# Performance work log

Measured on AMD Instinct MI355X. Metric: run time of the kernel, lower is better.

## Reference

```python
import jax, jax.numpy as jnp
import numpy as np
import math

N_HEAD = 16
N_EMBD = 1024
N_LATENTS = 64
HEAD_DIM = N_EMBD // N_HEAD  # 64
ROPE_THETA = 10000.0


def setup_inputs() -> dict:
    key = jax.random.key(0)
    ks = jax.random.split(key, 6)
    B, T = 4, 4096
    x = jax.random.normal(ks[0], (B, T, N_EMBD), dtype=jnp.float32)
    # torch Linear weights applied as x @ W with W: [in, out] (equivalent up to init)
    s = 1.0 / math.sqrt(N_EMBD)
    Wk = jax.random.normal(ks[1], (N_EMBD, N_EMBD), dtype=jnp.float32) * s
    Wv = jax.random.normal(ks[2], (N_EMBD, N_EMBD), dtype=jnp.float32) * s
    Wg = jax.random.normal(ks[3], (N_EMBD, N_HEAD * N_LATENTS), dtype=jnp.float32) * s
    Wp = jax.random.normal(ks[4], (N_EMBD, N_EMBD), dtype=jnp.float32) * s
    latent_q = jax.random.normal(ks[5], (1, N_LATENTS, N_HEAD, HEAD_DIM), dtype=jnp.float32)
    return {"x": x, "latent_q": latent_q, "Wk": Wk, "Wv": Wv, "Wg": Wg, "Wp": Wp}


def _rope_interleaved(k, theta):
    # k: [B, T, H, D]; interleaved pairs rotated by position-dependent angles
    B, T, H, D = k.shape
    inv_freq = 1.0 / (theta ** (jnp.arange(0, D, 2, dtype=jnp.float32) / D))  # [D/2]
    ang = jnp.arange(T, dtype=jnp.float32)[:, None] * inv_freq[None, :]       # [T, D/2]
    cos = jnp.cos(ang)[None, :, None, :]
    sin = jnp.sin(ang)[None, :, None, :]
    k2 = k.reshape(B, T, H, D // 2, 2)
    kr = jnp.stack([k2[..., 0] * cos - k2[..., 1] * sin,
                    k2[..., 0] * sin + k2[..., 1] * cos], axis=-1)
    return kr.reshape(B, T, H, D).astype(k.dtype)


def reference(x, latent_q, Wk, Wv, Wg, Wp):
    B, T, C = x.shape
    H, D, L = N_HEAD, HEAD_DIM, N_LATENTS
    k = (x @ Wk).reshape(B, T, H, D)
    v = (x @ Wv).reshape(B, T, H, D)
    gates = jax.nn.softmax((x @ Wg).reshape(B, T, H, L), axis=-1)  # [B,T,H,L]
    k = _rope_interleaved(k, ROPE_THETA)
    q = jnp.broadcast_to(latent_q, (B, L, H, D)).transpose(0, 2, 1, 3)  # [B,H,L,D]
    kt = k.transpose(0, 2, 1, 3)  # [B,H,T,D]
    vt = v.transpose(0, 2, 1, 3)  # [B,H,T,D]
    scale = 1.0 / jnp.sqrt(jnp.asarray(D, dtype=x.dtype))
    scores = jnp.einsum('bhld,bhtd->bhlt', q, kt) * scale  # [B,H,L,T]
    # PyTorch SDPA is_causal with L_q != L_kv: top-left aligned tril(ones(L, T))
    causal = jnp.arange(T)[None, :] <= jnp.arange(L)[:, None]  # [L,T]
    scores = jnp.where(causal[None, None], scores, -jnp.inf)
    attn = jax.nn.softmax(scores, axis=-1)
    attn_out = jnp.einsum('bhlt,bhtd->bhld', attn, vt)  # [B,H,L,D]
    gates_t = gates.transpose(0, 2, 1, 3)  # [B,H,T,L]
    weighted = jnp.einsum('bhld,bhtl->bhtd', attn_out, gates_t)  # [B,H,T,D]
    out = weighted.transpose(0, 2, 1, 3).reshape(B, T, C)
    return out @ Wp
```

## Files before the change

### kernel.cpp

```cpp
#include <hip/hip_runtime.h>
#include <hip/hip_bf16.h>


typedef __attribute__((ext_vector_type(8))) short bf16x8;
typedef __attribute__((ext_vector_type(4))) float f32x4;
typedef __attribute__((ext_vector_type(4))) unsigned short us4;

__device__ __forceinline__ void gll16(const void* g, void* l) {
  __builtin_amdgcn_global_load_lds((const __attribute__((address_space(1))) void*)g,
                                   (__attribute__((address_space(3))) void*)l, 16, 0, 0);
}

__global__ __launch_bounds__(256)
void prep_kernel(const float* __restrict__ x, __hip_bfloat16* __restrict__ xb,
                 const float* __restrict__ Wg, const float* __restrict__ Wk,
                 const float* __restrict__ Wv, const float* __restrict__ Wp,
                 __hip_bfloat16* __restrict__ WgT, __hip_bfloat16* __restrict__ WkT,
                 __hip_bfloat16* __restrict__ WvT, __hip_bfloat16* __restrict__ WpT) {
  const int bid = blockIdx.x, tid = threadIdx.x;
  if (bid < 2048) {
    const int stride = 2048 * 256;
    for (int i = bid * 256 + tid; i < 4194304; i += stride) {
      float4 f = reinterpret_cast<const float4*>(x)[i];
      union { __hip_bfloat16 h[4]; us4 v; } u;
      u.h[0] = __float2bfloat16(f.x);
      u.h[1] = __float2bfloat16(f.y);
      u.h[2] = __float2bfloat16(f.z);
      u.h[3] = __float2bfloat16(f.w);
      reinterpret_cast<us4*>(xb)[i] = u.v;
    }
  } else {
    const int t = bid - 2048;
    const int z = t >> 10, rem = t & 1023;
    const float* W = (z == 0) ? Wg : ((z == 1) ? Wk : ((z == 2) ? Wv : Wp));
    __hip_bfloat16* Wt = (z == 0) ? WgT : ((z == 1) ? WkT : ((z == 2) ? WvT : WpT));
    __shared__ float tile[32][33];
    const int bx = (rem & 31) * 32, by = (rem >> 5) * 32;
    const int tx = tid & 31, ty = tid >> 5;
    #pragma unroll
    for (int j = 0; j < 32; j += 8)
      tile[ty + j][tx] = W[(size_t)(by + ty + j) * 1024 + bx + tx];
    __syncthreads();
    #pragma unroll
    for (int j = 0; j < 32; j += 8)
      Wt[(size_t)(bx + ty + j) * 1024 + by + tx] = __float2bfloat16(tile[tx][ty + j]);
  }
}

template <int EPI>
__global__ __launch_bounds__(512, 2)
void gemm256(const __hip_bfloat16* __restrict__ A, const __hip_bfloat16* __restrict__ Bt,
             void* __restrict__ Cv, int K, int ldc,
             long long astride, long long bstride, long long cstride) {
  __shared__ __align__(16) unsigned short SA[2][256 * 64];
  __shared__ __align__(16) unsigned short SB[2][256 * 64];
  const int tid = threadIdx.x;
  const int lane = tid & 63;
  const int w = tid >> 6;
  const int wm = w >> 2, wn = w & 3;
  const int lr = lane & 15, lk = lane >> 4;
  const int m0 = blockIdx.x * 256, n0 = blockIdx.y * 256;
  const long long b = blockIdx.z;
  const __hip_bfloat16* Ab = A + b * astride;
  const __hip_bfloat16* Bb = Bt + b * bstride;

  f32x4 acc[8][4] = {};

  const int NT = K >> 6;
  int buf = 0;

  auto STAGE = [&](int bsel, int kt) {
    #pragma unroll
    for (int r = 0; r < 4; ++r) {
      int c = r * 512 + tid;
      int row = c >> 3, slot = c & 7;
      int gch = slot ^ (row & 7);
      gll16(Ab + (size_t)(m0 + row) * K + kt + gch * 8, (char*)&SA[bsel][0] + c * 16);
      gll16(Bb + (size_t)(n0 + row) * K + kt + gch * 8, (char*)&SB[bsel][0] + c * 16);
    }
  };

  STAGE(0, 0);
  __syncthreads();

  for (int t = 0; t < NT; ++t) {
    if (t + 1 < NT) STAGE(buf ^ 1, (t + 1) << 6);

    bf16x8 bfr[2][4];
    #pragma unroll
    for (int kk = 0; kk < 2; ++kk)
      #pragma unroll
      for (int ni = 0; ni < 4; ++ni) {
        int row = wn * 64 + ni * 16 + lr;
        int ch = (kk * 4 + lk) ^ (row & 7);
        bfr[kk][ni] = *(const bf16x8*)&SB[buf][row * 64 + ch * 8];
      }
    #pragma unroll
    for (int mi = 0; mi < 8; ++mi) {
      int row = wm * 128 + mi * 16 + lr;
      int ch0 = lk ^ (row & 7);
      int ch1 = (4 + lk) ^ (row & 7);
      bf16x8 a0 = *(const bf16x8*)&SA[buf][row * 64 + ch0 * 8];
      bf16x8 a1 = *(const bf16x8*)&SA[buf][row * 64 + ch1 * 8];
      #pragma unroll
      for (int ni = 0; ni < 4; ++ni)
        acc[mi][ni] = __builtin_amdgcn_mfma_f32_16x16x32_bf16(a0, bfr[0][ni], acc[mi][ni], 0, 0, 0);
      #pragma unroll
      for (int ni = 0; ni < 4; ++ni)
        acc[mi][ni] = __builtin_amdgcn_mfma_f32_16x16x32_bf16(a1, bfr[1][ni], acc[mi][ni], 0, 0, 0);
    }
    __syncthreads();
    buf ^= 1;
  }

  if (EPI == 0) {
    float* C = (float*)Cv + b * cstride;
    #pragma unroll
    for (int mi = 0; mi < 8; ++mi) {
      int r = m0 + wm * 128 + mi * 16 + lk * 4;
      #pragma unroll
      for (int ni = 0; ni < 4; ++ni) {
        int c = n0 + wn * 64 + ni * 16 + lr;
        #pragma unroll
        for (int jj = 0; jj < 4; ++jj)
          C[(size_t)(r + jj) * ldc + c] = acc[mi][ni][jj];
      }
    }
  } else {
    __hip_bfloat16* C = (__hip_bfloat16*)Cv + b * cstride;
    #pragma unroll
    for (int mi = 0; mi < 8; ++mi) {
      #pragma unroll
      for (int jj = 0; jj < 4; ++jj) {
        float mx = -3.0e38f;
        #pragma unroll
        for (int ni = 0; ni < 4; ++ni) mx = fmaxf(mx, acc[mi][ni][jj]);
        mx = fmaxf(mx, __shfl_xor(mx, 1));
        mx = fmaxf(mx, __shfl_xor(mx, 2));
        mx = fmaxf(mx, __shfl_xor(mx, 4));
        mx = fmaxf(mx, __shfl_xor(mx, 8));
        float e[4];
        float s = 0.f;
        #pragma unroll
        for (int ni = 0; ni < 4; ++ni) { e[ni] = __expf(acc[mi][ni][jj] - mx); s += e[ni]; }
        s += __shfl_xor(s, 1);
        s += __shfl_xor(s, 2);
        s += __shfl_xor(s, 4);
        s += __shfl_xor(s, 8);
        float inv = 1.0f / s;
        int r = m0 + wm * 128 + mi * 16 + lk * 4 + jj;
        #pragma unroll
        for (int ni = 0; ni < 4; ++ni)
          C[(size_t)r * ldc + n0 + wn * 64 + ni * 16 + lr] = __float2bfloat16(e[ni] * inv);
      }
    }
  }
}

__global__ __launch_bounds__(256)
void gemm_kv(const __hip_bfloat16* __restrict__ A, const __hip_bfloat16* __restrict__ Bt,
             float* __restrict__ kvp) {
  __shared__ __align__(16) unsigned short As[128 * 32];
  __shared__ __align__(16) unsigned short Bs[128 * 32];
  const int tid = threadIdx.x;
  const int lane = tid & 63;
  const int w = tid >> 6;
  const int wm = w >> 1, wn = w & 1;
  const int lr = lane & 15, lk = lane >> 4;
  const int m0 = blockIdx.x * 128, n0 = blockIdx.y * 128;
  const int ks = blockIdx.z;
  const int K = 1024;

  f32x4 acc[4][4] = {};
  const int r0 = tid >> 2;
  const int c8 = (tid & 3) * 8;

  auto xrow = [&](int rg) { return (size_t)(rg >> 6) * 4096 + (rg & 63); };

  for (int ki = 0; ki < 4; ++ki) {
    int kt = ks * 128 + ki * 32;
    __syncthreads();
    gll16(A + xrow(m0 + r0) * K + kt + c8,      (char*)As + (w * 64) * 16);
    gll16(Bt + (size_t)(n0 + r0) * K + kt + c8, (char*)Bs + (w * 64) * 16);
    gll16(A + xrow(m0 + 64 + r0) * K + kt + c8,      (char*)As + (256 + w * 64) * 16);
    gll16(Bt + (size_t)(n0 + 64 + r0) * K + kt + c8, (char*)Bs + (256 + w * 64) * 16);
    __syncthreads();

    bf16x8 af[4], bf[4];
    #pragma unroll
    for (int mi = 0; mi < 4; ++mi)
      af[mi] = *(const bf16x8*)&As[(wm * 64 + mi * 16 + lr) * 32 + lk * 8];
    #pragma unroll
    for (int ni = 0; ni < 4; ++ni)
      bf[ni] = *(const bf16x8*)&Bs[(wn * 64 + ni * 16 + lr) * 32 + lk * 8];
    #pragma unroll
    for (int mi = 0; mi < 4; ++mi)
      #pragma unroll
      for (int ni = 0; ni < 4; ++ni)
        acc[mi][ni] = __builtin_amdgcn_mfma_f32_16x16x32_bf16(af[mi], bf[ni], acc[mi][ni], 0, 0, 0);
  }

  float* C = kvp + (size_t)ks * 256 * 2048;
  #pragma unroll
  for (int mi = 0; mi < 4; ++mi) {
    int r = m0 + wm * 64 + mi * 16 + lk * 4;
    #pragma unroll
    for (int ni = 0; ni < 4; ++ni) {
      int c = n0 + wn * 64 + ni * 16 + lr;
      #pragma unroll
      for (int jj = 0; jj < 4; ++jj)
        C[(size_t)(r + jj) * 2048 + c] = acc[mi][ni][jj];
    }
  }
}

__global__ __launch_bounds__(256)
void attn_mt(const float* __restrict__ kvp, const float* __restrict__ lq,
             const __hip_bfloat16* __restrict__ WpT, __hip_bfloat16* __restrict__ Mt) {
  const int ct = blockIdx.x, h = blockIdx.y, b = blockIdx.z;
  __shared__ float Ks[64][64];
  __shared__ float Vs[64][64];
  __shared__ float S[64][65];
  __shared__ float Pt[64][65];
  __shared__ __align__(16) unsigned short SW[256 * 64];
  __shared__ __align__(16) unsigned short SAo[64 * 64];
  const int tid = threadIdx.x;
  const int lane = tid & 63;
  const int w = tid >> 6;
  const int lr = lane & 15, lk = lane >> 4;

  #pragma unroll
  for (int j = 0; j < 8; ++j) {
    int c2 = j * 256 + tid;
    int row = c2 >> 3, slot = c2 & 7;
    int gch = slot ^ (row & 7);
    gll16(WpT + (size_t)(ct * 256 + row) * 1024 + h * 64 + gch * 8, (char*)SW + c2 * 16);
  }

  {
    int r = tid >> 4;
    int c4 = (tid & 15) * 4;
    int i0 = c4 >> 1;
    float inv0 = exp2f(-13.287712379549449f * ((float)i0 * (1.0f / 32.0f)));
    float inv1 = exp2f(-13.287712379549449f * ((float)(i0 + 1) * (1.0f / 32.0f)));
    #pragma unroll
    for (int j = 0; j < 4; ++j) {
      int row = j * 16 + r;
      float4 kf = make_float4(0.f, 0.f, 0.f, 0.f);
      float4 vf = make_float4(0.f, 0.f, 0.f, 0.f);
      #pragma unroll
      for (int ks = 0; ks < 8; ++ks) {
        const float* base = kvp + ((size_t)ks * 256 + b * 64 + row) * 2048 + h * 64;
        float4 kp = *(const float4*)(base + c4);
        float4 vp = *(const float4*)(base + 1024 + c4);
        kf.x += kp.x; kf.y += kp.y; kf.z += kp.z; kf.w += kp.w;
        vf.x += vp.x; vf.y += vp.y; vf.z += vp.z; vf.w += vp.w;
      }
      float a0 = (float)row * inv0, a1 = (float)row * inv1;
      float s0 = sinf(a0), c0 = cosf(a0), s1 = sinf(a1), c1 = cosf(a1);
      *(float4*)&Ks[row][c4] = make_float4(kf.x * c0 - kf.y * s0, kf.x * s0 + kf.y * c0,
                                           kf.z * c1 - kf.w * s1, kf.z * s1 + kf.w * c1);
      *(float4*)&Vs[row][c4] = vf;
    }
  }
  __syncthreads();

  {
    const int l = tid & 63;
    float q[64];
    const float4* lq4 = (const float4*)(lq + ((size_t)l * 16 + h) * 64);
    #pragma unroll
    for (int i = 0; i < 16; ++i) {
      float4 f = lq4[i];
      q[4 * i] = f.x; q[4 * i + 1] = f.y; q[4 * i + 2] = f.z; q[4 * i + 3] = f.w;
    }
    #pragma unroll
    for (int tl = 0; tl < 16; ++tl) {
      int t = w * 16 + tl;
      float a = 0.f;
      #pragma unroll
      for (int d4 = 0; d4 < 16; ++d4) {
        float4 kf = *(const float4*)&Ks[t][d4 * 4];
        a += q[4 * d4] * kf.x + q[4 * d4 + 1] * kf.y + q[4 * d4 + 2] * kf.z + q[4 * d4 + 3] * kf.w;
      }
      S[l][t] = a * 0.125f;
    }
  }
  __syncthreads();

  {
    const int l = tid >> 2, c = tid & 3;
    float sv[16];
    float mx = -3.0e38f;
    #pragma unroll
    for (int i = 0; i < 16; ++i) {
      int t = c * 16 + i;
      sv[i] = S[l][t];
      if (t <= l) mx = fmaxf(mx, sv[i]);
    }
    mx = fmaxf(mx, __shfl_xor(mx, 1));
    mx = fmaxf(mx, __shfl_xor(mx, 2));
    float sum = 0.f;
    float e[16];
    #pragma unroll
    for (int i = 0; i < 16; ++i) {
      int t = c * 16 + i;
      e[i] = (t <= l) ? __expf(sv[i] - mx) : 0.f;
      sum += e[i];
    }
    sum += __shfl_xor(sum, 1);
    sum += __shfl_xor(sum, 2);
    float inv = 1.0f / sum;
    #pragma unroll
    for (int i = 0; i < 16; ++i) Pt[c * 16 + i][l] = e[i] * inv;
  }
  __syncthreads();

  {
    const int l = tid & 63;
    float o[16];
    #pragma unroll
    for (int i = 0; i < 16; ++i) o[i] = 0.f;
    for (int t = 0; t < 64; ++t) {
      float p = Pt[t][l];
      #pragma unroll
      for (int d4 = 0; d4 < 4; ++d4) {
        float4 vf = *(const float4*)&Vs[t][w * 16 + d4 * 4];
        o[4 * d4]     += p * vf.x;
        o[4 * d4 + 1] += p * vf.y;
        o[4 * d4 + 2] += p * vf.z;
        o[4 * d4 + 3] += p * vf.w;
      }
    }
    union { __hip_bfloat16 hh[8]; bf16x8 v; } p0, p1;
    #pragma unroll
    for (int i = 0; i < 8; ++i) { p0.hh[i] = __float2bfloat16(o[i]); p1.hh[i] = __float2bfloat16(o[8 + i]); }
    *(bf16x8*)&SAo[l * 64 + ((2 * w) ^ (l & 7)) * 8]     = p0.v;
    *(bf16x8*)&SAo[l * 64 + ((2 * w + 1) ^ (l & 7)) * 8] = p1.v;
  }
  __syncthreads();

  f32x4 acc[4][4] = {};
  bf16x8 bfr[2][4];
  #pragma unroll
  for (int kk = 0; kk < 2; ++kk)
    #pragma unroll
    for (int ni = 0; ni < 4; ++ni) {
      int row = ni * 16 + lr;
      int ch = (kk * 4 + lk) ^ (row & 7);
      bfr[kk][ni] = *(const bf16x8*)&SAo[row * 64 + ch * 8];
    }
  #pragma unroll
  for (int mi = 0; mi < 4; ++mi) {
    int row = w * 64 + mi * 16 + lr;
    int ch0 = lk ^ (row & 7);
    int ch1 = (4 + lk) ^ (row & 7);
    bf16x8 a0 = *(const bf16x8*)&SW[row * 64 + ch0 * 8];
    bf16x8 a1 = *(const bf16x8*)&SW[row * 64 + ch1 * 8];
    #pragma unroll
    for (int ni = 0; ni < 4; ++ni)
      acc[mi][ni] = __builtin_amdgcn_mfma_f32_16x16x32_bf16(a0, bfr[0][ni], acc[mi][ni], 0, 0, 0);
    #pragma unroll
    for (int ni = 0; ni < 4; ++ni)
      acc[mi][ni] = __builtin_amdgcn_mfma_f32_16x16x32_bf16(a1, bfr[1][ni], acc[mi][ni], 0, 0, 0);
  }

  #pragma unroll
  for (int mi = 0; mi < 4; ++mi) {
    int c = ct * 256 + w * 64 + mi * 16 + lk * 4;
    #pragma unroll
    for (int ni = 0; ni < 4; ++ni) {
      int l = ni * 16 + lr;
      #pragma unroll
      for (int jj = 0; jj < 4; ++jj)
        Mt[((size_t)b * 1024 + c + jj) * 1024 + h * 64 + l] = __float2bfloat16(acc[mi][ni][jj]);
    }
  }
}

extern "C" void kernel_launch(void* const* d_in, const int* in_sizes, int n_in,
                              void* d_out, int out_size, void* d_ws, size_t ws_size,
                              hipStream_t stream) {
  const float* x  = (const float*)d_in[0];
  const float* lq = (const float*)d_in[1];
  const float* Wk = (const float*)d_in[2];
  const float* Wv = (const float*)d_in[3];
  const float* Wg = (const float*)d_in[4];
  const float* Wp = (const float*)d_in[5];
  float* out = (float*)d_out;

  char* w = (char*)d_ws;
  __hip_bfloat16* xb   = (__hip_bfloat16*)(w);
  __hip_bfloat16* G    = (__hip_bfloat16*)(w + 33554432);
  __hip_bfloat16* WgT  = (__hip_bfloat16*)(w + 67108864);
  __hip_bfloat16* WkvT = (__hip_bfloat16*)(w + 69206016);
  __hip_bfloat16* WpT  = (__hip_bfloat16*)(w + 73400320);
  __hip_bfloat16* Mt   = (__hip_bfloat16*)(w + 75497472);
  float* kvp = out;

  prep_kernel<<<6144, 256, 0, stream>>>(x, xb, Wg, Wk, Wv, Wp,
                                        WgT, WkvT, WkvT + 1024 * 1024, WpT);

  gemm256<1><<<dim3(64, 4, 1), 512, 0, stream>>>(xb, WgT, G, 1024, 1024, 0LL, 0LL, 0LL);

  gemm_kv<<<dim3(2, 16, 8), 256, 0, stream>>>(xb, WkvT, kvp);

  attn_mt<<<dim3(4, 16, 4), 256, 0, stream>>>(kvp, lq, WpT, Mt);

  gemm256<0><<<dim3(16, 4, 4), 512, 0, stream>>>(G, Mt, out, 1024, 1024,
                                                 4096LL * 1024, 1024LL * 1024, 4096LL * 1024);
}
```

Baseline: 135.2 us.

## Fuse K/V projection of first 64 tokens into attention kernel

```diff
diff --git a/kernel.cpp b/kernel.cpp
--- a/kernel.cpp
+++ b/kernel.cpp
@@ -158,72 +158,18 @@
 }
 
 __global__ __launch_bounds__(256)
-void gemm_kv(const __hip_bfloat16* __restrict__ A, const __hip_bfloat16* __restrict__ Bt,
-             float* __restrict__ kvp) {
-  __shared__ __align__(16) unsigned short As[128 * 32];
-  __shared__ __align__(16) unsigned short Bs[128 * 32];
-  const int tid = threadIdx.x;
-  const int lane = tid & 63;
-  const int w = tid >> 6;
-  const int wm = w >> 1, wn = w & 1;
-  const int lr = lane & 15, lk = lane >> 4;
-  const int m0 = blockIdx.x * 128, n0 = blockIdx.y * 128;
-  const int ks = blockIdx.z;
-  const int K = 1024;
-
-  f32x4 acc[4][4] = {};
-  const int r0 = tid >> 2;
-  const int c8 = (tid & 3) * 8;
-
-  auto xrow = [&](int rg) { return (size_t)(rg >> 6) * 4096 + (rg & 63); };
-
-  for (int ki = 0; ki < 4; ++ki) {
-    int kt = ks * 128 + ki * 32;
-    __syncthreads();
-    gll16(A + xrow(m0 + r0) * K + kt + c8,      (char*)As + (w * 64) * 16);
-    gll16(Bt + (size_t)(n0 + r0) * K + kt + c8, (char*)Bs + (w * 64) * 16);
-    gll16(A + xrow(m0 + 64 + r0) * K + kt + c8,      (char*)As + (256 + w * 64) * 16);
-    gll16(Bt + (size_t)(n0 + 64 + r0) * K + kt + c8, (char*)Bs + (256 + w * 64) * 16);
-    __syncthreads();
-
-    bf16x8 af[4], bf[4];
-    #pragma unroll
-    for (int mi = 0; mi < 4; ++mi)
-      af[mi] = *(const bf16x8*)&As[(wm * 64 + mi * 16 + lr) * 32 + lk * 8];
-    #pragma unroll
-    for (int ni = 0; ni < 4; ++ni)
-      bf[ni] = *(const bf16x8*)&Bs[(wn * 64 + ni * 16 + lr) * 32 + lk * 8];
-    #pragma unroll
-    for (int mi = 0; mi < 4; ++mi)
-      #pragma unroll
-      for (int ni = 0; ni < 4; ++ni)
-        acc[mi][ni] = __builtin_amdgcn_mfma_f32_16x16x32_bf16(af[mi], bf[ni], acc[mi][ni], 0, 0, 0);
-  }
-
-  float* C = kvp + (size_t)ks * 256 * 2048;
-  #pragma unroll
-  for (int mi = 0; mi < 4; ++mi) {
-    int r = m0 + wm * 64 + mi * 16 + lk * 4;
-    #pragma unroll
-    for (int ni = 0; ni < 4; ++ni) {
-      int c = n0 + wn * 64 + ni * 16 + lr;
-      #pragma unroll
-      for (int jj = 0; jj < 4; ++jj)
-        C[(size_t)(r + jj) * 2048 + c] = acc[mi][ni][jj];
-    }
-  }
-}
-
-__global__ __launch_bounds__(256)
-void attn_mt(const float* __restrict__ kvp, const float* __restrict__ lq,
-             const __hip_bfloat16* __restrict__ WpT, __hip_bfloat16* __restrict__ Mt) {
+void attn_mt(const float* __restrict__ X, const float* __restrict__ lq,
+             const __hip_bfloat16* __restrict__ WkvT, const __hip_bfloat16* __restrict__ WpT,
+             __hip_bfloat16* __restrict__ Mt) {
   const int ct = blockIdx.x, h = blockIdx.y, b = blockIdx.z;
+  __shared__ __align__(16) unsigned short XA[64 * 32];
+  __shared__ __align__(16) unsigned short BB[128 * 32];
+  __shared__ __align__(16) unsigned short SW[256 * 64];
+  __shared__ __align__(16) unsigned short SAo[64 * 64];
   __shared__ float Ks[64][64];
   __shared__ float Vs[64][64];
   __shared__ float S[64][65];
   __shared__ float Pt[64][65];
-  __shared__ __align__(16) unsigned short SW[256 * 64];
-  __shared__ __align__(16) unsigned short SAo[64 * 64];
   const int tid = threadIdx.x;
   const int lane = tid & 63;
   const int w = tid >> 6;
@@ -237,30 +183,69 @@
     gll16(WpT + (size_t)(ct * 256 + row) * 1024 + h * 64 + gch * 8, (char*)SW + c2 * 16);
   }
 
-  {
-    int r = tid >> 4;
-    int c4 = (tid & 15) * 4;
-    int i0 = c4 >> 1;
-    float inv0 = exp2f(-13.287712379549449f * ((float)i0 * (1.0f / 32.0f)));
-    float inv1 = exp2f(-13.287712379549449f * ((float)(i0 + 1) * (1.0f / 32.0f)));
-    #pragma unroll
-    for (int j = 0; j < 4; ++j) {
-      int row = j * 16 + r;
-      float4 kf = make_float4(0.f, 0.f, 0.f, 0.f);
-      float4 vf = make_float4(0.f, 0.f, 0.f, 0.f);
-      #pragma unroll
-      for (int ks = 0; ks < 8; ++ks) {
-        const float* base = kvp + ((size_t)ks * 256 + b * 64 + row) * 2048 + h * 64;
-        float4 kp = *(const float4*)(base + c4);
-        float4 vp = *(const float4*)(base + 1024 + c4);
-        kf.x += kp.x; kf.y += kp.y; kf.z += kp.z; kf.w += kp.w;
-        vf.x += vp.x; vf.y += vp.y; vf.z += vp.z; vf.w += vp.w;
-      }
-      float a0 = (float)row * inv0, a1 = (float)row * inv1;
-      float s0 = sinf(a0), c0 = cosf(a0), s1 = sinf(a1), c1 = cosf(a1);
-      *(float4*)&Ks[row][c4] = make_float4(kf.x * c0 - kf.y * s0, kf.x * s0 + kf.y * c0,
-                                           kf.z * c1 - kf.w * s1, kf.z * s1 + kf.w * c1);
-      *(float4*)&Vs[row][c4] = vf;
+  f32x4 pacc[4][2] = {};
+  {
+    const float* xb_ = X + (size_t)b * 4096 * 1024;
+    const int xrow = tid >> 2, xslot = tid & 3;
+    for (int kt = 0; kt < 1024; kt += 32) {
+      __syncthreads();
+      {
+        const float* src = xb_ + (size_t)xrow * 1024 + kt + xslot * 8;
+        float4 a0 = *(const float4*)src;
+        float4 a1 = *(const float4*)(src + 4);
+        union { __hip_bfloat16 hh[8]; bf16x8 v; } p;
+        p.hh[0] = __float2bfloat16(a0.x); p.hh[1] = __float2bfloat16(a0.y);
+        p.hh[2] = __float2bfloat16(a0.z); p.hh[3] = __float2bfloat16(a0.w);
+        p.hh[4] = __float2bfloat16(a1.x); p.hh[5] = __float2bfloat16(a1.y);
+        p.hh[6] = __float2bfloat16(a1.z); p.hh[7] = __float2bfloat16(a1.w);
+        *(bf16x8*)&XA[xrow * 32 + xslot * 8] = p.v;
+      }
+      #pragma unroll
+      for (int r = 0; r < 2; ++r) {
+        int c = r * 256 + tid;
+        int row = c >> 2, slot = c & 3;
+        const __hip_bfloat16* src = (row < 64)
+            ? WkvT + (size_t)(h * 64 + row) * 1024
+            : WkvT + 1048576 + (size_t)(h * 64 + row - 64) * 1024;
+        gll16(src + kt + slot * 8, (char*)BB + c * 16);
+      }
+      __syncthreads();
+
+      bf16x8 bf0 = *(const bf16x8*)&BB[(w * 32 + lr) * 32 + lk * 8];
+      bf16x8 bf1 = *(const bf16x8*)&BB[(w * 32 + 16 + lr) * 32 + lk * 8];
+      #pragma unroll
+      for (int mi = 0; mi < 4; ++mi) {
+        bf16x8 af = *(const bf16x8*)&XA[(mi * 16 + lr) * 32 + lk * 8];
+        pacc[mi][0] = __builtin_amdgcn_mfma_f32_16x16x32_bf16(af, bf0, pacc[mi][0], 0, 0, 0);
+        pacc[mi][1] = __builtin_amdgcn_mfma_f32_16x16x32_bf16(af, bf1, pacc[mi][1], 0, 0, 0);
+      }
+    }
+  }
+  #pragma unroll
+  for (int mi = 0; mi < 4; ++mi)
+    #pragma unroll
+    for (int ni = 0; ni < 2; ++ni) {
+      int c = w * 32 + ni * 16 + lr;
+      #pragma unroll
+      for (int jj = 0; jj < 4; ++jj) {
+        int t = mi * 16 + lk * 4 + jj;
+        if (w < 2) Ks[t][c] = pacc[mi][ni][jj];
+        else       Vs[t][c - 64] = pacc[mi][ni][jj];
+      }
+    }
+  __syncthreads();
+
+  {
+    const int pi = tid & 31;
+    const float inv = exp2f(-13.287712379549449f * ((float)pi * (1.0f / 32.0f)));
+    #pragma unroll
+    for (int j = 0; j < 8; ++j) {
+      int t = (tid >> 5) + 8 * j;
+      float ang = (float)t * inv;
+      float s = sinf(ang), c = cosf(ang);
+      float k0 = Ks[t][2 * pi], k1 = Ks[t][2 * pi + 1];
+      Ks[t][2 * pi]     = k0 * c - k1 * s;
+      Ks[t][2 * pi + 1] = k0 * s + k1 * c;
     }
   }
   __syncthreads();
@@ -396,16 +381,13 @@
   __hip_bfloat16* WkvT = (__hip_bfloat16*)(w + 69206016);
   __hip_bfloat16* WpT  = (__hip_bfloat16*)(w + 73400320);
   __hip_bfloat16* Mt   = (__hip_bfloat16*)(w + 75497472);
-  float* kvp = out;
 
   prep_kernel<<<6144, 256, 0, stream>>>(x, xb, Wg, Wk, Wv, Wp,
                                         WgT, WkvT, WkvT + 1024 * 1024, WpT);
 
   gemm256<1><<<dim3(64, 4, 1), 512, 0, stream>>>(xb, WgT, G, 1024, 1024, 0LL, 0LL, 0LL);
 
-  gemm_kv<<<dim3(2, 16, 8), 256, 0, stream>>>(xb, WkvT, kvp);
-
-  attn_mt<<<dim3(4, 16, 4), 256, 0, stream>>>(kvp, lq, WpT, Mt);
+  attn_mt<<<dim3(4, 16, 4), 256, 0, stream>>>(x, lq, WkvT, WpT, Mt);
 
   gemm256<0><<<dim3(16, 4, 4), 512, 0, stream>>>(G, Mt, out, 1024, 1024,
                                                  4096LL * 1024, 1024LL * 1024, 4096LL * 1024);
```

Result: slower. 139.3 us (+3.0%).
